# Optimization experiments

Hardware: AMD Instinct MI355X
Metric: run time of the kernel (lower is better)

Reference implementation:

```python
import jax, jax.numpy as jnp
import numpy as np

SCALE = 0.1
TEMP = 1.0
LN_EPS = 1e-6
NORM_EPS = 1e-12  # torch F.normalize eps

def setup_inputs() -> dict:
    key = jax.random.key(0)
    k1, = jax.random.split(key, 1)
    x = jax.random.normal(k1, (8192, 512), dtype=jnp.float32)
    gamma = jnp.ones((512,), dtype=jnp.float32)
    beta = jnp.zeros((512,), dtype=jnp.float32)
    return {"x": x, "gamma": gamma, "beta": beta}

def reference(x, gamma, beta):
    # L2-normalize rows (torch F.normalize semantics: x / max(||x||, eps))
    norm = jnp.maximum(jnp.linalg.norm(x, axis=1, keepdims=True), NORM_EPS)
    xn = x / norm                                   # [N, d]
    sim = (xn @ xn.T) / TEMP                        # [N, N]
    # dual_norm: row softmax + column softmax
    sim = jax.nn.softmax(sim, axis=1) + jax.nn.softmax(sim, axis=0)
    x_neg = sim @ x                                 # [N, d]
    y = x - SCALE * x_neg
    # LayerNorm over last dim, eps=1e-6
    mean = jnp.mean(y, axis=-1, keepdims=True)
    var = jnp.mean(jnp.square(y - mean), axis=-1, keepdims=True)
    out = (y - mean) * jax.lax.rsqrt(var + LN_EPS) * gamma + beta
    return out
```

## Files before the change

kernel.cpp:

```cpp
#include <hip/hip_runtime.h>
#include <math.h>

#define NN 8192
#define DD 512

constexpr float SCALE_C = 0.1f;
constexpr float LN_EPS_C = 1e-6f;
constexpr float NORM_EPS_C = 1e-12f;
constexpr float CBIG = 32768.0f;
constexpr float INV_CBIG = 1.0f / 32768.0f;

typedef __attribute__((ext_vector_type(8))) short bf16x8;
typedef __attribute__((ext_vector_type(4))) float f32x4;

#define MFMA16(a, b, c) __builtin_amdgcn_mfma_f32_16x16x32_bf16((a), (b), (c), 0, 0, 0)
#define MFMA8(a, b, c)                                                        \
  __builtin_amdgcn_mfma_f32_16x16x32_fp8_fp8((long)(a), (long)(b), (c), 0, 0, 0)

#define GLL16(g, l)                                                        \
  __builtin_amdgcn_global_load_lds(                                        \
      (const __attribute__((address_space(1))) unsigned int*)(g),          \
      (__attribute__((address_space(3))) unsigned int*)(l), 16, 0, 0)

#define WAITV4() asm volatile("s_waitcnt vmcnt(4)" ::: "memory")
#define WAITV0() asm volatile("s_waitcnt vmcnt(0)" ::: "memory")
#define WAITLGKM0() asm volatile("s_waitcnt lgkmcnt(0)" ::: "memory")
#define FENCE() asm volatile("" ::: "memory")
#define BAR() __builtin_amdgcn_s_barrier()

__device__ inline unsigned short f2bf(float f) {
  unsigned int u = __builtin_bit_cast(unsigned int, f);
  unsigned int r = (u + 0x7FFFu + ((u >> 16) & 1u)) >> 16;
  return (unsigned short)r;
}

__device__ inline unsigned int f2fp8n(float f) {
  unsigned int a = __builtin_bit_cast(unsigned int, f);
  unsigned int r = a + 0x7FFFFu + ((a >> 20) & 1u);
  return (r >> 20) - 960u;
}

__device__ inline unsigned int f2fp8(float f) {
  unsigned int u = __builtin_bit_cast(unsigned int, f);
  unsigned int s = (u >> 24) & 0x80u;
  unsigned int a = u & 0x7fffffffu;
  if (a >= 0x3C800000u) {
    unsigned int r = a + 0x7FFFFu + ((a >> 20) & 1u);
    return s | ((r >> 20) - 960u);
  }
  float af = __builtin_bit_cast(float, a);
  return s | (unsigned int)(int)rintf(af * 512.0f);
}

__device__ inline float fp82f(unsigned int b) {
  return __builtin_bit_cast(float, (b + 960u) << 20);
}

__global__ __launch_bounds__(256) void k_prep2(const float* __restrict__ x,
                                               unsigned short* __restrict__ xnb,
                                               unsigned char* __restrict__ xT8) {
  __shared__ unsigned int T8w[16][130];
  const int j0 = blockIdx.x * 16;
  const int t = threadIdx.x;
  const int tr = t >> 4, tc = t & 15;
  const int row = j0 + tr;
  const float* xr = x + (size_t)row * DD;
  float4 v[8];
  float ss = 0.f;
#pragma unroll
  for (int k = 0; k < 8; ++k) {
    v[k] = *(const float4*)(xr + tc * 4 + k * 64);
    ss += v[k].x * v[k].x + v[k].y * v[k].y + v[k].z * v[k].z + v[k].w * v[k].w;
  }
#pragma unroll
  for (int off = 1; off < 16; off <<= 1) ss += __shfl_xor(ss, off);
  const float rn = 1.0f / fmaxf(sqrtf(ss), NORM_EPS_C);
#pragma unroll
  for (int k = 0; k < 8; ++k) {
    ushort4 o;
    o.x = f2bf(v[k].x * rn);
    o.y = f2bf(v[k].y * rn);
    o.z = f2bf(v[k].z * rn);
    o.w = f2bf(v[k].w * rn);
    *(ushort4*)(xnb + (size_t)row * DD + tc * 4 + k * 64) = o;
    T8w[tr][tc + k * 16] = f2fp8(v[k].x) | (f2fp8(v[k].y) << 8) |
                           (f2fp8(v[k].z) << 16) | (f2fp8(v[k].w) << 24);
  }
  __syncthreads();
#pragma unroll
  for (int q = 0; q < 2; ++q) {
    const int d = t + q * 256;
    const unsigned char* col = (const unsigned char*)&T8w[0][0] + d;
    unsigned int wds[4];
#pragma unroll
    for (int p = 0; p < 4; ++p)
      wds[p] = (unsigned int)col[(p * 4 + 0) * 520] |
               ((unsigned int)col[(p * 4 + 1) * 520] << 8) |
               ((unsigned int)col[(p * 4 + 2) * 520] << 16) |
               ((unsigned int)col[(p * 4 + 3) * 520] << 24);
    *(uint4*)&xT8[(size_t)d * NN + j0] = make_uint4(wds[0], wds[1], wds[2], wds[3]);
  }
}

__global__ __launch_bounds__(256, 4) void k_rowsumE(const unsigned short* __restrict__ xnb,
                                                    float* __restrict__ lpart,
                                                    unsigned char* __restrict__ E8) {
  __shared__ __align__(16) unsigned char POOL[32768];
  __shared__ float red[4][64];
  __shared__ float red2[4][64];

  int b = blockIdx.x, bi = 0;
  while (b >= 64 - bi) { b -= 64 - bi; ++bi; }
  const int bj = bi + b;
  const int i0 = bi * 128, j0 = bj * 128;
  const int diag = (bi == bj);

  const int t = threadIdx.x;
  const int w = t >> 6, l = t & 63;
  const int lr = l & 15, lg = l >> 4;
  const int wr = w >> 1, wc = w & 1;
  const int r0 = w * 16 + (l >> 2);
  const int clog = (l & 3) ^ ((r0 >> 1) & 3);
  const unsigned short* gA = xnb + (size_t)(i0 + r0) * DD + clog * 8;
  const unsigned short* gB = xnb + (size_t)(j0 + r0) * DD + clog * 8;

#define RS_STAGE(s, koff)                                                        \
  do {                                                                           \
    GLL16(gA + (koff), (unsigned short*)(POOL + (s) * 16384) + w * 512);         \
    GLL16(gA + (size_t)64 * DD + (koff),                                         \
          (unsigned short*)(POOL + (s) * 16384 + 4096) + w * 512);               \
    GLL16(gB + (koff), (unsigned short*)(POOL + (s) * 16384 + 8192) + w * 512);  \
    GLL16(gB + (size_t)64 * DD + (koff),                                         \
          (unsigned short*)(POOL + (s) * 16384 + 12288) + w * 512);              \
  } while (0)

  RS_STAGE(0, 0);
  RS_STAGE(1, 32);

  f32x4 acc[4][4] = {};
  for (int ks = 0; ks < 16; ++ks) {
    if (ks + 1 < 16) { WAITV4(); } else { WAITV0(); }
    BAR(); FENCE();
    const char* AS = (const char*)(POOL + (ks & 1) * 16384);
    const char* BS = AS + 8192;
    bf16x8 af[4], bv[4];
#pragma unroll
    for (int fm = 0; fm < 4; ++fm) {
      const int row = wr * 64 + fm * 16 + lr;
      af[fm] = *(const bf16x8*)(AS + row * 64 + ((lg ^ ((row >> 1) & 3)) << 4));
    }
#pragma unroll
    for (int fn = 0; fn < 4; ++fn) {
      const int row = wc * 64 + fn * 16 + lr;
      bv[fn] = *(const bf16x8*)(BS + row * 64 + ((lg ^ ((row >> 1) & 3)) << 4));
    }
    WAITLGKM0();
    BAR(); FENCE();
    if (ks + 2 < 16) RS_STAGE(ks & 1, (size_t)(ks + 2) * 32);
#pragma unroll
    for (int fm = 0; fm < 4; ++fm)
#pragma unroll
      for (int fn = 0; fn < 4; ++fn)
        acc[fm][fn] = MFMA16(af[fm], bv[fn], acc[fm][fn]);
  }

  unsigned int ebw[4][4];
  float rsum[4][4] = {};
  float csum[4] = {};
#pragma unroll
  for (int fm = 0; fm < 4; ++fm)
#pragma unroll
    for (int fn = 0; fn < 4; ++fn) {
      unsigned int pw = 0;
#pragma unroll
      for (int rr = 0; rr < 4; ++rr) {
        float e = __expf(acc[fm][fn][rr]);
        rsum[fm][rr] += e;
        csum[fn] += e;
        pw |= f2fp8n(e) << (8 * rr);
      }
      ebw[fm][fn] = pw;
    }

#pragma unroll
  for (int fm = 0; fm < 4; ++fm)
#pragma unroll
    for (int rr = 0; rr < 4; ++rr) {
      float s = rsum[fm][rr];
#pragma unroll
      for (int off = 1; off < 16; off <<= 1) s += __shfl_xor(s, off);
      if (lr == 0) red[w][fm * 16 + lg * 4 + rr] = s;
    }
  if (!diag) {
#pragma unroll
    for (int fn = 0; fn < 4; ++fn) {
      float cs = csum[fn];
      cs += __shfl_xor(cs, 16);
      cs += __shfl_xor(cs, 32);
      if (lg == 0) red2[w][fn * 16 + lr] = cs;
    }
  }

  unsigned char(*Et2)[144] = (unsigned char(*)[144])POOL;
#pragma unroll
  for (int fm = 0; fm < 4; ++fm)
#pragma unroll
    for (int fn = 0; fn < 4; ++fn)
      *(unsigned int*)&Et2[wc * 64 + fn * 16 + lr][wr * 64 + fm * 16 + lg * 4] =
          ebw[fm][fn];
  __syncthreads();
  {
    unsigned char* dst2 = E8 + ((size_t)(bj * 64 + bi) << 14);
#pragma unroll
    for (int q = 0; q < 4; ++q) {
      const int f = t + q * 256;
      *(uint4*)(dst2 + f * 16) = *(const uint4*)&Et2[f >> 3][(f & 7) * 16];
    }
  }
  if (t < 128) {
    const int wrx = t >> 6, idx = t & 63;
    lpart[(size_t)bj * NN + i0 + t] = red[2 * wrx][idx] + red[2 * wrx + 1][idx];
  } else if (!diag) {
    const int c = t - 128;
    const int wcx = c >> 6, idx = c & 63;
    lpart[(size_t)bi * NN + j0 + c] = red2[wcx][idx] + red2[2 + wcx][idx];
  }
}

__global__ __launch_bounds__(256) void k_recip(const float* __restrict__ lpart,
                                               float* __restrict__ rl) {
  const int i = blockIdx.x * 256 + threadIdx.x;
  float s = 0.f;
  for (int c = 0; c < 64; ++c) s += lpart[(size_t)c * NN + i];
  rl[i] = CBIG / s;
}

__global__ __launch_bounds__(256) void k_scale2(unsigned char* __restrict__ P,
                                                const float* __restrict__ rl) {
  __shared__ unsigned int T32[128][35];
  int b = blockIdx.x, ti = 0;
  while (b >= 64 - ti) { b -= 64 - ti; ++ti; }
  const int tj = ti + b;
  const int i0 = ti * 128, j0 = tj * 128;
  const int t = threadIdx.x;
  unsigned char* tileC = P + ((size_t)(tj * 64 + ti) << 14);

#pragma unroll
  for (int q = 0; q < 4; ++q) {
    const int f = t + q * 256;
    const int r = f >> 3;
    const int c0 = (f & 7) * 16;
    uint4 v = *(const uint4*)(tileC + f * 16);
    const float rlr = rl[j0 + r];
    float rlc[16];
#pragma unroll
    for (int p = 0; p < 4; ++p) {
      float4 r4 = *(const float4*)(rl + i0 + c0 + p * 4);
      rlc[p * 4 + 0] = r4.x; rlc[p * 4 + 1] = r4.y;
      rlc[p * 4 + 2] = r4.z; rlc[p * 4 + 3] = r4.w;
    }
    unsigned int wsrc[4] = {v.x, v.y, v.z, v.w};
    unsigned int wdst[4];
#pragma unroll
    for (int p = 0; p < 4; ++p) {
      unsigned int in = wsrc[p], out = 0;
#pragma unroll
      for (int k = 0; k < 4; ++k) {
        float e = fp82f((in >> (8 * k)) & 0xffu);
        out |= f2fp8n(e * (rlr + rlc[p * 4 + k])) << (8 * k);
      }
      wdst[p] = out;
      T32[r][(c0 >> 2) + p] = out;
    }
    *(uint4*)(tileC + f * 16) = make_uint4(wdst[0], wdst[1], wdst[2], wdst[3]);
  }
  if (ti == tj) return;
  __syncthreads();

  unsigned char* tileT = P + ((size_t)(ti * 64 + tj) << 14);
  {
    const int rg = t >> 3;
    const int cc = t & 7;
    const int c2 = cc * 16;
    unsigned int o[4][4];
#pragma unroll
    for (int k4 = 0; k4 < 4; ++k4) {
      unsigned int a0 = T32[c2 + k4 * 4 + 0][rg];
      unsigned int a1 = T32[c2 + k4 * 4 + 1][rg];
      unsigned int a2 = T32[c2 + k4 * 4 + 2][rg];
      unsigned int a3 = T32[c2 + k4 * 4 + 3][rg];
      unsigned int b0 = (a0 & 0x00FF00FFu) | ((a1 << 8) & 0xFF00FF00u);
      unsigned int b1 = ((a0 >> 8) & 0x00FF00FFu) | (a1 & 0xFF00FF00u);
      unsigned int b2 = (a2 & 0x00FF00FFu) | ((a3 << 8) & 0xFF00FF00u);
      unsigned int b3 = ((a2 >> 8) & 0x00FF00FFu) | (a3 & 0xFF00FF00u);
      o[0][k4] = (b0 & 0x0000FFFFu) | (b2 << 16);
      o[1][k4] = (b1 & 0x0000FFFFu) | (b3 << 16);
      o[2][k4] = (b0 >> 16) | (b2 & 0xFFFF0000u);
      o[3][k4] = (b1 >> 16) | (b3 & 0xFFFF0000u);
    }
#pragma unroll
    for (int i = 0; i < 4; ++i)
      *(uint4*)(tileT + (size_t)(rg * 4 + i) * 128 + c2) =
          make_uint4(o[i][0], o[i][1], o[i][2], o[i][3]);
  }
}

__global__ __launch_bounds__(256, 4) void k_pv3(const unsigned char* __restrict__ P8,
                                                const unsigned char* __restrict__ xT8,
                                                unsigned short* __restrict__ parts) {
  __shared__ __align__(16) unsigned char POOL[34816];
  const int i0 = blockIdx.x * 128;
  const int n0 = blockIdx.y * 128;
  const int z = blockIdx.z;
  const int t = threadIdx.x;
  const int w = t >> 6, l = t & 63;
  const int lr = l & 15, lg = l >> 4;
  const int wr = w >> 1, wc = w & 1;
  const int r0 = w * 16 + (l >> 2);
  const int clog = (l & 3) ^ ((r0 >> 1) & 3);
  const unsigned char* Abase = P8 + ((size_t)((i0 >> 7) * 64 + z * 16) << 14) +
                               r0 * 128 + clog * 16;
  const unsigned char* gB = xT8 + (size_t)(n0 + r0) * NN + z * 2048 + clog * 16;

#define PV_STAGE(s, koff)                                                      \
  do {                                                                         \
    const unsigned char* a_ = Abase + (((koff) >> 7) << 14) + ((koff) & 127);  \
    GLL16(a_, POOL + (s) * 8192 + w * 1024);                                   \
    GLL16(a_ + 8192, POOL + (s) * 8192 + 4096 + w * 1024);                     \
    GLL16(gB + (koff), POOL + 16384 + (s) * 8192 + w * 1024);                  \
    GLL16(gB + (size_t)64 * NN + (koff),                                       \
          POOL + 16384 + (s) * 8192 + 4096 + w * 1024);                        \
  } while (0)

  PV_STAGE(0, 0);
  PV_STAGE(1, 64);

  f32x4 acc[4][4] = {};
  for (int ks = 0; ks < 32; ++ks) {
    if (ks + 1 < 32) { WAITV4(); } else { WAITV0(); }
    BAR(); FENCE();
    const char* AS = (const char*)(POOL + (ks & 1) * 8192);
    const char* BS = (const char*)(POOL + 16384 + (ks & 1) * 8192);
    unsigned long long af[4][2], bv[4][2];
#pragma unroll
    for (int fm = 0; fm < 4; ++fm) {
      const int row = wr * 64 + fm * 16 + lr;
      const int swz = (row >> 1) & 3;
#pragma unroll
      for (int kk = 0; kk < 2; ++kk) {
        int off = row * 64 + (((kk * 2 + (lg >> 1)) ^ swz) << 4) + ((lg & 1) << 3);
        af[fm][kk] = *(const unsigned long long*)(AS + off);
      }
    }
#pragma unroll
    for (int fn = 0; fn < 4; ++fn) {
      const int row = wc * 64 + fn * 16 + lr;
      const int swz = (row >> 1) & 3;
#pragma unroll
      for (int kk = 0; kk < 2; ++kk) {
        int off = row * 64 + (((kk * 2 + (lg >> 1)) ^ swz) << 4) + ((lg & 1) << 3);
        bv[fn][kk] = *(const unsigned long long*)(BS + off);
      }
    }
    WAITLGKM0();
    BAR(); FENCE();
    if (ks + 2 < 32) PV_STAGE(ks & 1, (ks + 2) * 64);
#pragma unroll
    for (int kk = 0; kk < 2; ++kk)
#pragma unroll
      for (int fm = 0; fm < 4; ++fm)
#pragma unroll
        for (int fn = 0; fn < 4; ++fn)
          acc[fm][fn] = MFMA8(af[fm][kk], bv[fn][kk], acc[fm][fn]);
  }

  BAR(); FENCE();
  unsigned short* Pt = (unsigned short*)POOL;
#pragma unroll
  for (int fm = 0; fm < 4; ++fm)
#pragma unroll
    for (int fn = 0; fn < 4; ++fn) {
      const int col = wc * 64 + fn * 16 + lr;
#pragma unroll
      for (int rr = 0; rr < 4; ++rr) {
        const int row = wr * 64 + fm * 16 + lg * 4 + rr;
        Pt[row * 136 + col] = f2bf(acc[fm][fn][rr] * INV_CBIG);
      }
    }
  __syncthreads();
  {
    unsigned short* dst = parts + (size_t)z * NN * DD + (size_t)i0 * DD + n0;
#pragma unroll
    for (int q = 0; q < 8; ++q) {
      const int f = t + q * 256;
      const int row = f >> 4, ch = f & 15;
      *(uint4*)(dst + (size_t)row * DD + ch * 8) =
          *(const uint4*)&Pt[row * 136 + ch * 8];
    }
  }
}

__global__ __launch_bounds__(256) void k_ln(const float* __restrict__ x,
                                            float* __restrict__ out,
                                            const unsigned short* __restrict__ parts,
                                            const float* __restrict__ gamma,
                                            const float* __restrict__ beta) {
  const int row = blockIdx.x * 4 + (threadIdx.x >> 6);
  const int l = threadIdx.x & 63;
  const int c0 = l * 8;

  float p[8] = {};
#pragma unroll
  for (int s = 0; s < 4; ++s) {
    uint4 q = *(const uint4*)(parts + (size_t)s * NN * DD + (size_t)row * DD + c0);
    unsigned int wq[4] = {q.x, q.y, q.z, q.w};
#pragma unroll
    for (int j = 0; j < 4; ++j) {
      p[2 * j + 0] += __builtin_bit_cast(float, wq[j] << 16);
      p[2 * j + 1] += __builtin_bit_cast(float, wq[j] & 0xFFFF0000u);
    }
  }
  float4 xv0 = *(const float4*)(x + (size_t)row * DD + c0);
  float4 xv1 = *(const float4*)(x + (size_t)row * DD + c0 + 4);
  float y[8];
  y[0] = xv0.x - SCALE_C * p[0];
  y[1] = xv0.y - SCALE_C * p[1];
  y[2] = xv0.z - SCALE_C * p[2];
  y[3] = xv0.w - SCALE_C * p[3];
  y[4] = xv1.x - SCALE_C * p[4];
  y[5] = xv1.y - SCALE_C * p[5];
  y[6] = xv1.z - SCALE_C * p[6];
  y[7] = xv1.w - SCALE_C * p[7];

  float sum = 0.f;
#pragma unroll
  for (int j = 0; j < 8; ++j) sum += y[j];
#pragma unroll
  for (int off = 1; off < 64; off <<= 1) sum += __shfl_xor(sum, off);
  const float mean = sum * (1.0f / DD);

  float d[8], vs = 0.f;
#pragma unroll
  for (int j = 0; j < 8; ++j) {
    d[j] = y[j] - mean;
    vs += d[j] * d[j];
  }
#pragma unroll
  for (int off = 1; off < 64; off <<= 1) vs += __shfl_xor(vs, off);
  const float rstd = rsqrtf(vs * (1.0f / DD) + LN_EPS_C);

  float4 g0 = *(const float4*)(gamma + c0);
  float4 g1 = *(const float4*)(gamma + c0 + 4);
  float4 b0 = *(const float4*)(beta + c0);
  float4 b1 = *(const float4*)(beta + c0 + 4);
  float4 o0, o1;
  o0.x = d[0] * rstd * g0.x + b0.x;
  o0.y = d[1] * rstd * g0.y + b0.y;
  o0.z = d[2] * rstd * g0.z + b0.z;
  o0.w = d[3] * rstd * g0.w + b0.w;
  o1.x = d[4] * rstd * g1.x + b1.x;
  o1.y = d[5] * rstd * g1.y + b1.y;
  o1.z = d[6] * rstd * g1.z + b1.z;
  o1.w = d[7] * rstd * g1.w + b1.w;
  *(float4*)(out + (size_t)row * DD + c0) = o0;
  *(float4*)(out + (size_t)row * DD + c0 + 4) = o1;
}

extern "C" void kernel_launch(void* const* d_in, const int* in_sizes, int n_in,
                              void* d_out, int out_size, void* d_ws, size_t ws_size,
                              hipStream_t stream) {
  const float* x = (const float*)d_in[0];
  const float* gamma = (const float*)d_in[1];
  const float* beta = (const float*)d_in[2];
  float* out = (float*)d_out;

  unsigned short* xnb = (unsigned short*)d_ws;
  unsigned char* xT8 = (unsigned char*)(xnb + (size_t)NN * DD);
  float* lpart = (float*)(xT8 + (size_t)NN * DD);
  float* rl = lpart + (size_t)64 * NN;
  unsigned short* parts = (unsigned short*)(rl + NN);
  unsigned char* E8 = (unsigned char*)(parts + (size_t)4 * NN * DD);

  k_prep2<<<NN / 16, 256, 0, stream>>>(x, xnb, xT8);
  k_rowsumE<<<2080, 256, 0, stream>>>(xnb, lpart, E8);
  k_recip<<<NN / 256, 256, 0, stream>>>(lpart, rl);
  k_scale2<<<2080, 256, 0, stream>>>(E8, rl);
  k_pv3<<<dim3(64, 4, 4), 256, 0, stream>>>(E8, xT8, parts);
  k_ln<<<NN / 4, 256, 0, stream>>>(x, out, parts, gamma, beta);
}
```

Before: 147.5 us.

## Enlarge similarity-exp kernel tiles to 256x256 with 512 threads and deeper K steps

The row-sum/exp kernel now computes 256x256 output tiles per block with 8 waves instead of 128x128 with 4 waves. It stages 64-wide K slices, using a double-buffered 128KB LDS pool with an XOR swizzle, and raises wave priority around the MFMA bursts. Each tile's exponentials and partial row/column sums are split back into the existing 128-granular E8 and lpart layout. The aim is to roughly halve global and LDS operand traffic per MFMA. The trade-off is that LDS use limits the kernel to one block per CU, and the 528-block grid leaves a small tail wave.

```diff
diff --git a/kernel.cpp b/kernel.cpp
--- a/kernel.cpp
+++ b/kernel.cpp
@@ -102,73 +102,92 @@
   }
 }
 
-__global__ __launch_bounds__(256, 4) void k_rowsumE(const unsigned short* __restrict__ xnb,
+__global__ __launch_bounds__(512, 2) void k_rowsumE(const unsigned short* __restrict__ xnb,
                                                     float* __restrict__ lpart,
                                                     unsigned char* __restrict__ E8) {
-  __shared__ __align__(16) unsigned char POOL[32768];
-  __shared__ float red[4][64];
-  __shared__ float red2[4][64];
-
-  int b = blockIdx.x, bi = 0;
-  while (b >= 64 - bi) { b -= 64 - bi; ++bi; }
-  const int bj = bi + b;
-  const int i0 = bi * 128, j0 = bj * 128;
-  const int diag = (bi == bj);
+  __shared__ __align__(16) unsigned char POOL[131072];
+
+  int b = blockIdx.x, BI = 0;
+  while (b >= 32 - BI) { b -= 32 - BI; ++BI; }
+  const int BJ = BI + b;
+  const int i0 = BI * 256, j0 = BJ * 256;
+  const int diag = (BI == BJ);
 
   const int t = threadIdx.x;
   const int w = t >> 6, l = t & 63;
   const int lr = l & 15, lg = l >> 4;
-  const int wr = w >> 1, wc = w & 1;
-  const int r0 = w * 16 + (l >> 2);
-  const int clog = (l & 3) ^ ((r0 >> 1) & 3);
-  const unsigned short* gA = xnb + (size_t)(i0 + r0) * DD + clog * 8;
-  const unsigned short* gB = xnb + (size_t)(j0 + r0) * DD + clog * 8;
-
-#define RS_STAGE(s, koff)                                                        \
-  do {                                                                           \
-    GLL16(gA + (koff), (unsigned short*)(POOL + (s) * 16384) + w * 512);         \
-    GLL16(gA + (size_t)64 * DD + (koff),                                         \
-          (unsigned short*)(POOL + (s) * 16384 + 4096) + w * 512);               \
-    GLL16(gB + (koff), (unsigned short*)(POOL + (s) * 16384 + 8192) + w * 512);  \
-    GLL16(gB + (size_t)64 * DD + (koff),                                         \
-          (unsigned short*)(POOL + (s) * 16384 + 12288) + w * 512);              \
+  const int wr = w >> 2, wc = w & 3;
+
+#define ST_HALF(Rglob, LbOff, ktv)                                             \
+  do {                                                                         \
+    _Pragma("unroll") for (int q_ = 0; q_ < 2; ++q_) {                         \
+      const int f_ = q_ * 512 + t;                                             \
+      const int row_ = f_ >> 3, c_ = f_ & 7;                                   \
+      GLL16((const unsigned char*)xnb + (size_t)((Rglob) + row_) * 1024 +      \
+                (ktv) * 128 + ((c_ ^ (row_ & 7)) << 4),                        \
+            POOL + (LbOff) + q_ * 8192 + w * 1024);                            \
+    }                                                                          \
   } while (0)
 
-  RS_STAGE(0, 0);
-  RS_STAGE(1, 32);
-
-  f32x4 acc[4][4] = {};
-  for (int ks = 0; ks < 16; ++ks) {
-    if (ks + 1 < 16) { WAITV4(); } else { WAITV0(); }
+  ST_HALF(i0, 0, 0);
+  ST_HALF(i0 + 128, 16384, 0);
+  ST_HALF(j0, 32768, 0);
+  ST_HALF(j0 + 128, 49152, 0);
+
+  f32x4 acc[8][4] = {};
+
+  for (int kt = 0; kt < 8; ++kt) {
+    const int buf = kt & 1;
+    const unsigned char* Ab = POOL + buf * 65536;
+    const unsigned char* Bb = Ab + 32768;
+    WAITV0();
     BAR(); FENCE();
-    const char* AS = (const char*)(POOL + (ks & 1) * 16384);
-    const char* BS = AS + 8192;
-    bf16x8 af[4], bv[4];
-#pragma unroll
-    for (int fm = 0; fm < 4; ++fm) {
-      const int row = wr * 64 + fm * 16 + lr;
-      af[fm] = *(const bf16x8*)(AS + row * 64 + ((lg ^ ((row >> 1) & 3)) << 4));
-    }
+    if (kt + 1 < 8) {
+      const int nb = (buf ^ 1) * 65536;
+      ST_HALF(i0, nb + 0, kt + 1);
+      ST_HALF(i0 + 128, nb + 16384, kt + 1);
+      ST_HALF(j0, nb + 32768, kt + 1);
+      ST_HALF(j0 + 128, nb + 49152, kt + 1);
+    }
+    bf16x8 bv[4][2];
 #pragma unroll
     for (int fn = 0; fn < 4; ++fn) {
       const int row = wc * 64 + fn * 16 + lr;
-      bv[fn] = *(const bf16x8*)(BS + row * 64 + ((lg ^ ((row >> 1) & 3)) << 4));
-    }
-    WAITLGKM0();
-    BAR(); FENCE();
-    if (ks + 2 < 16) RS_STAGE(ks & 1, (size_t)(ks + 2) * 32);
-#pragma unroll
-    for (int fm = 0; fm < 4; ++fm)
-#pragma unroll
-      for (int fn = 0; fn < 4; ++fn)
-        acc[fm][fn] = MFMA16(af[fm], bv[fn], acc[fm][fn]);
-  }
-
-  unsigned int ebw[4][4];
-  float rsum[4][4] = {};
+#pragma unroll
+      for (int kk = 0; kk < 2; ++kk)
+        bv[fn][kk] = *(const bf16x8*)(Bb + row * 128 +
+                                      (((kk * 4 + lg) ^ (row & 7)) << 4));
+    }
+#pragma unroll
+    for (int p = 0; p < 4; ++p) {
+      bf16x8 af[2][2];
+#pragma unroll
+      for (int fq = 0; fq < 2; ++fq) {
+        const int row = wr * 128 + (2 * p + fq) * 16 + lr;
+#pragma unroll
+        for (int kk = 0; kk < 2; ++kk)
+          af[fq][kk] = *(const bf16x8*)(Ab + row * 128 +
+                                        (((kk * 4 + lg) ^ (row & 7)) << 4));
+      }
+      __builtin_amdgcn_s_setprio(1);
+#pragma unroll
+      for (int kk = 0; kk < 2; ++kk)
+#pragma unroll
+        for (int fq = 0; fq < 2; ++fq)
+#pragma unroll
+          for (int fn = 0; fn < 4; ++fn)
+            acc[2 * p + fq][fn] =
+                MFMA16(af[fq][kk], bv[fn][kk], acc[2 * p + fq][fn]);
+      __builtin_amdgcn_s_setprio(0);
+    }
+  }
+  BAR(); FENCE();
+
+  unsigned int ebw[8][4];
+  float rsum[8][4] = {};
   float csum[4] = {};
 #pragma unroll
-  for (int fm = 0; fm < 4; ++fm)
+  for (int fm = 0; fm < 8; ++fm)
 #pragma unroll
     for (int fn = 0; fn < 4; ++fn) {
       unsigned int pw = 0;
@@ -182,14 +201,16 @@
       ebw[fm][fn] = pw;
     }
 
-#pragma unroll
-  for (int fm = 0; fm < 4; ++fm)
+  float* redrow = (float*)(POOL + 69632);
+  float* redcol = (float*)(POOL + 73728);
+#pragma unroll
+  for (int fm = 0; fm < 8; ++fm)
 #pragma unroll
     for (int rr = 0; rr < 4; ++rr) {
       float s = rsum[fm][rr];
 #pragma unroll
       for (int off = 1; off < 16; off <<= 1) s += __shfl_xor(s, off);
-      if (lr == 0) red[w][fm * 16 + lg * 4 + rr] = s;
+      if (lr == 0) redrow[(wr * 4 + wc) * 128 + fm * 16 + lg * 4 + rr] = s;
     }
   if (!diag) {
 #pragma unroll
@@ -197,33 +218,45 @@
       float cs = csum[fn];
       cs += __shfl_xor(cs, 16);
       cs += __shfl_xor(cs, 32);
-      if (lg == 0) red2[w][fn * 16 + lr] = cs;
-    }
-  }
-
-  unsigned char(*Et2)[144] = (unsigned char(*)[144])POOL;
-#pragma unroll
-  for (int fm = 0; fm < 4; ++fm)
+      if (lg == 0) redcol[wr * 256 + wc * 64 + fn * 16 + lr] = cs;
+    }
+  }
+
+  unsigned char(*Et2)[264] = (unsigned char(*)[264])POOL;
+#pragma unroll
+  for (int fm = 0; fm < 8; ++fm)
 #pragma unroll
     for (int fn = 0; fn < 4; ++fn)
-      *(unsigned int*)&Et2[wc * 64 + fn * 16 + lr][wr * 64 + fm * 16 + lg * 4] =
+      *(unsigned int*)&Et2[wc * 64 + fn * 16 + lr][wr * 128 + fm * 16 + lg * 4] =
           ebw[fm][fn];
   __syncthreads();
-  {
-    unsigned char* dst2 = E8 + ((size_t)(bj * 64 + bi) << 14);
-#pragma unroll
-    for (int q = 0; q < 4; ++q) {
-      const int f = t + q * 256;
-      *(uint4*)(dst2 + f * 16) = *(const uint4*)&Et2[f >> 3][(f & 7) * 16];
-    }
-  }
-  if (t < 128) {
-    const int wrx = t >> 6, idx = t & 63;
-    lpart[(size_t)bj * NN + i0 + t] = red[2 * wrx][idx] + red[2 * wrx + 1][idx];
+
+#pragma unroll
+  for (int a = 0; a < 2; ++a)
+#pragma unroll
+    for (int bq = 0; bq < 2; ++bq) {
+      unsigned char* dst =
+          E8 + ((size_t)((2 * BJ + bq) * 64 + (2 * BI + a)) << 14);
+#pragma unroll
+      for (int q = 0; q < 2; ++q) {
+        const int f = q * 512 + t;
+        const int rr_ = f >> 3, cc_ = (f & 7) * 16;
+        *(uint4*)(dst + f * 16) =
+            *(const uint4*)&Et2[bq * 128 + rr_][a * 128 + cc_];
+      }
+    }
+  if (t < 256) {
+    const int row = t & 127, wrx = t >> 7;
+    const float h0 = redrow[(wrx * 4 + 0) * 128 + row] +
+                     redrow[(wrx * 4 + 1) * 128 + row];
+    const float h1 = redrow[(wrx * 4 + 2) * 128 + row] +
+                     redrow[(wrx * 4 + 3) * 128 + row];
+    lpart[(size_t)(2 * BJ) * NN + i0 + wrx * 128 + row] = h0;
+    lpart[(size_t)(2 * BJ + 1) * NN + i0 + wrx * 128 + row] = h1;
   } else if (!diag) {
-    const int c = t - 128;
-    const int wcx = c >> 6, idx = c & 63;
-    lpart[(size_t)bi * NN + j0 + c] = red2[wcx][idx] + red2[2 + wcx][idx];
+    const int col = t - 256;
+    const float tot = redcol[col] + redcol[256 + col];
+    lpart[(size_t)(2 * BI + (col >> 7)) * NN + j0 + col] = tot;
   }
 }
 
@@ -482,7 +515,7 @@
   unsigned char* E8 = (unsigned char*)(parts + (size_t)4 * NN * DD);
 
   k_prep2<<<NN / 16, 256, 0, stream>>>(x, xnb, xT8);
-  k_rowsumE<<<2080, 256, 0, stream>>>(xnb, lpart, E8);
+  k_rowsumE<<<528, 512, 0, stream>>>(xnb, lpart, E8);
   k_recip<<<NN / 256, 256, 0, stream>>>(lpart, rl);
   k_scale2<<<2080, 256, 0, stream>>>(E8, rl);
   k_pv3<<<dim3(64, 4, 4), 256, 0, stream>>>(E8, xT8, parts);
```

Result: slower. 167.6 us (+13.6%).
